# Kernel tuning notes

Measured on AMD Instinct MI355X. Metric: run time of the kernel, lower is better.

## Reference

```python
import jax, jax.numpy as jnp
import numpy as np

H = 1024  # projected hidden size per branch


def setup_inputs() -> dict:
    key = jax.random.key(0)
    ks = jax.random.split(key, 8)
    B, E, D, F = 8, 1024, 1024, 768
    s = 1.0 / np.sqrt(F)
    return {
        "encoder_last_hidden_state": jax.random.normal(ks[0], (B, E, F), jnp.float32),
        "decoder_hidden_states": jax.random.normal(ks[1], (1, B, D, F), jnp.float32),
        "encoder_mask": jnp.ones((B, E), jnp.float32),
        "decoder_mask": jnp.ones((B, D), jnp.float32),
        "W_e": jax.random.normal(ks[2], (H, F), jnp.float32) * s,
        "b_e": jnp.zeros((H,), jnp.float32),
        "W_d": jax.random.normal(ks[3], (H, F), jnp.float32) * s,
        "b_d": jnp.zeros((H,), jnp.float32),
        "W1": jax.random.normal(ks[4], (3, 2 * H), jnp.float32) * (1.0 / np.sqrt(2 * H)),
        "b1": jnp.zeros((3,), jnp.float32),
        "grid_label": jax.random.randint(ks[5], (B, D, E), 0, 3, jnp.int64),
    }


def reference(encoder_last_hidden_state, decoder_hidden_states, encoder_mask,
              decoder_mask, W_e, b_e, W_d, b_d, W1, b1, grid_label):
    # dropout is identity in eval mode
    dec_hs = decoder_hidden_states[-1]                      # (B, D, 768)
    enc_s = jax.nn.relu(encoder_last_hidden_state @ W_e.T + b_e) * encoder_mask[:, :, None]  # (B,E,H)
    dec_s = jax.nn.relu(dec_hs @ W_d.T + b_d) * decoder_mask[:, :, None]                     # (B,D,H)
    # layer_1 on cat([decode, encode], -1) == split GEMMs + broadcast add
    W1_d, W1_e = W1[:, :H], W1[:, H:]
    d_proj = dec_s @ W1_d.T                                 # (B, D, 3)
    e_proj = enc_s @ W1_e.T                                 # (B, E, 3)
    logits = d_proj[:, :, None, :] + e_proj[:, None, :, :] + b1  # (B, D, E, 3)
    logp = jax.nn.log_softmax(logits, axis=-1)
    valid = grid_label != -100
    safe = jnp.where(valid, grid_label, 0)
    nll = -jnp.take_along_axis(logp, safe[..., None].astype(jnp.int32), axis=-1)[..., 0]
    denom = jnp.maximum(jnp.sum(valid.astype(logp.dtype)), 1.0)
    return jnp.sum(jnp.where(valid, nll, 0.0)) / denom
```

## Files before the change

kernel.cpp:

```cpp
#include <hip/hip_runtime.h>
#include <hip/hip_bf16.h>

typedef __attribute__((ext_vector_type(8))) __bf16 bf16x8;
typedef __attribute__((ext_vector_type(4))) float f32x4;

#define HID 1024
#define FD  768
#define MR  8192
#define BM  128
#define BN  128
#define BK  32
#define KSTEPS (FD / BK)

#define GLOAD_LDS16(g, l)                                                  \
    __builtin_amdgcn_global_load_lds(                                      \
        (const __attribute__((address_space(1))) unsigned int*)(g),        \
        (__attribute__((address_space(3))) unsigned int*)(l), 16, 0, 0)

__global__ __launch_bounds__(256)
void cvt_kernel(const float* __restrict__ se, const float* __restrict__ sd,
                const float* __restrict__ swe, const float* __restrict__ swd,
                __bf16* __restrict__ de, __bf16* __restrict__ dd,
                __bf16* __restrict__ dwe, __bf16* __restrict__ dwd)
{
    const int blk = blockIdx.x;
    const float* __restrict__ src;
    __bf16* __restrict__ dst;
    long base;
    if (blk < 3072)      { src = se;  dst = de;  base = (long)blk * 2048; }
    else if (blk < 6144) { src = sd;  dst = dd;  base = (long)(blk - 3072) * 2048; }
    else if (blk < 6528) { src = swe; dst = dwe; base = (long)(blk - 6144) * 2048; }
    else                 { src = swd; dst = dwd; base = (long)(blk - 6528) * 2048; }
    const long i = base + (long)threadIdx.x * 8;
    const float4 a = *reinterpret_cast<const float4*>(src + i);
    const float4 b = *reinterpret_cast<const float4*>(src + i + 4);
    bf16x8 w;
    w[0] = (__bf16)a.x; w[1] = (__bf16)a.y; w[2] = (__bf16)a.z; w[3] = (__bf16)a.w;
    w[4] = (__bf16)b.x; w[5] = (__bf16)b.y; w[6] = (__bf16)b.z; w[7] = (__bf16)b.w;
    *reinterpret_cast<bf16x8*>(dst + i) = w;
}

__global__ __launch_bounds__(256)
void gemm_proj_kernel(const __bf16* __restrict__ Xe, const __bf16* __restrict__ Xd,
                      const __bf16* __restrict__ We, const __bf16* __restrict__ Wd,
                      const float* __restrict__ me, const float* __restrict__ md,
                      const float* __restrict__ be, const float* __restrict__ bd,
                      const float* __restrict__ W1,
                      float* __restrict__ pe, float* __restrict__ pd)
{
    const int z = blockIdx.z;
    const __bf16* __restrict__ X    = z ? Xd : Xe;
    const __bf16* __restrict__ Wt   = z ? Wd : We;
    const float* __restrict__ bias  = z ? bd : be;
    const float* __restrict__ msk   = z ? md : me;
    float* __restrict__ proj        = z ? pd : pe;
    const int w1off = z ? 0 : HID;

    __shared__ union {
        struct { __bf16 A[2][BM][BK]; __bf16 B[2][BN][BK]; } st;
        f32x4 red[BM][16];
    } sm;

    const int t    = threadIdx.x;
    const int lane = t & 63;
    const int wid  = t >> 6;
    const int wr   = wid >> 1;
    const int wc   = wid & 1;
    const int l15  = lane & 15;
    const int l4   = lane >> 4;

    const long m0 = (long)blockIdx.x * BM;
    const int  n0 = blockIdx.y * BN;

    f32x4 acc[4][4];
    #pragma unroll
    for (int i = 0; i < 4; ++i)
        #pragma unroll
        for (int j = 0; j < 4; ++j)
            acc[i][j] = (f32x4){0.f, 0.f, 0.f, 0.f};

    const int srow = lane >> 2;
    const int scol = (lane & 3) * 8;
    const __bf16* ga = X  + (m0 + wid*32 + srow) * (long)FD + scol;
    const __bf16* gb = Wt + (long)(n0 + wid*32 + srow) * FD + scol;

#define STAGE(p, ks) do {                                                  \
        const int k0_ = (ks) * BK;                                         \
        GLOAD_LDS16(ga + k0_,               &sm.st.A[p][wid*32 +  0][0]);  \
        GLOAD_LDS16(ga + (long)16*FD + k0_, &sm.st.A[p][wid*32 + 16][0]);  \
        GLOAD_LDS16(gb + k0_,               &sm.st.B[p][wid*32 +  0][0]);  \
        GLOAD_LDS16(gb + (long)16*FD + k0_, &sm.st.B[p][wid*32 + 16][0]);  \
    } while (0)

    STAGE(0, 0);
    __syncthreads();

    int cur = 0;
    for (int ks = 0; ks < KSTEPS; ++ks) {
        if (ks + 1 < KSTEPS) STAGE(cur ^ 1, ks + 1);

        bf16x8 af[4], bfr[4];
        #pragma unroll
        for (int m = 0; m < 4; ++m)
            af[m] = *reinterpret_cast<const bf16x8*>(&sm.st.A[cur][wr*64 + m*16 + l15][l4*8]);
        #pragma unroll
        for (int n = 0; n < 4; ++n)
            bfr[n] = *reinterpret_cast<const bf16x8*>(&sm.st.B[cur][wc*64 + n*16 + l15][l4*8]);

        #pragma unroll
        for (int m = 0; m < 4; ++m)
            #pragma unroll
            for (int n = 0; n < 4; ++n)
                acc[m][n] = __builtin_amdgcn_mfma_f32_16x16x32_bf16(
                                af[m], bfr[n], acc[m][n], 0, 0, 0);

        __syncthreads();
        cur ^= 1;
    }

    float bh[4], w1c0[4], w1c1[4], w1c2[4];
    #pragma unroll
    for (int n = 0; n < 4; ++n) {
        int h = n0 + wc*64 + n*16 + l15;
        bh[n]   = bias[h];
        w1c0[n] = W1[0*2*HID + w1off + h];
        w1c1[n] = W1[1*2*HID + w1off + h];
        w1c2[n] = W1[2*2*HID + w1off + h];
    }

    #pragma unroll
    for (int pass = 0; pass < 2; ++pass) {
        if (wc == pass) {
            #pragma unroll
            for (int m = 0; m < 4; ++m) {
                #pragma unroll
                for (int r = 0; r < 4; ++r) {
                    float p0 = 0.f, p1 = 0.f, p2 = 0.f;
                    #pragma unroll
                    for (int n = 0; n < 4; ++n) {
                        float s = fmaxf(acc[m][n][r] + bh[n], 0.f);
                        p0 = fmaf(s, w1c0[n], p0);
                        p1 = fmaf(s, w1c1[n], p1);
                        p2 = fmaf(s, w1c2[n], p2);
                    }
                    const int row = wr*64 + m*16 + l4*4 + r;
                    f32x4 v = (f32x4){p0, p1, p2, 0.f};
                    if (pass == 0) sm.red[row][l15] = v;
                    else           sm.red[row][l15] = sm.red[row][l15] + v;
                }
            }
        }
        __syncthreads();
    }

    {
        const int rrow = t >> 1, half = t & 1;
        f32x4 s = (f32x4){0.f, 0.f, 0.f, 0.f};
        #pragma unroll
        for (int j = 0; j < 8; ++j)
            s = s + sm.red[rrow][half*8 + ((j + rrow) & 7)];
        s.x += __shfl_xor(s.x, 1);
        s.y += __shfl_xor(s.y, 1);
        s.z += __shfl_xor(s.z, 1);
        if (half == 0) {
            const long grow = m0 + rrow;
            const float mk = msk[grow];
            atomicAdd(&proj[grow*3+0], s.x * mk);
            atomicAdd(&proj[grow*3+1], s.y * mk);
            atomicAdd(&proj[grow*3+2], s.z * mk);
        }
    }
#undef STAGE
}

__global__ __launch_bounds__(256)
void loss_kernel(const float* __restrict__ pe, const float* __restrict__ pd,
                 const float* __restrict__ b1, const int* __restrict__ labels,
                 float* __restrict__ psum, float* __restrict__ pcnt)
{
    const int g = blockIdx.x;
    const int b = g >> 8;
    const int dbase = (g & 255) * 4;
    const int t = threadIdx.x;
    const int e0 = t * 4;

    const float4* pep = reinterpret_cast<const float4*>(pe + ((long)b*1024 + e0)*3);
    float4 q0 = pep[0], q1 = pep[1], q2 = pep[2];
    float epv[12] = {q0.x,q0.y,q0.z,q0.w, q1.x,q1.y,q1.z,q1.w, q2.x,q2.y,q2.z,q2.w};

    float lsum = 0.f, lcnt = 0.f;
    #pragma unroll
    for (int r = 0; r < 4; ++r) {
        const long bd = (long)b*1024 + dbase + r;
        const float d0 = pd[bd*3+0] + b1[0];
        const float d1 = pd[bd*3+1] + b1[1];
        const float d2 = pd[bd*3+2] + b1[2];
        const int4 lb = *reinterpret_cast<const int4*>(labels + bd*1024 + e0);
        const int lv[4] = {lb.x, lb.y, lb.z, lb.w};
        #pragma unroll
        for (int i = 0; i < 4; ++i) {
            float l0 = d0 + epv[i*3+0];
            float l1 = d1 + epv[i*3+1];
            float l2 = d2 + epv[i*3+2];
            float mx  = fmaxf(l0, fmaxf(l1, l2));
            float lse = mx + __logf(__expf(l0-mx) + __expf(l1-mx) + __expf(l2-mx));
            int la = lv[i];
            if (la != -100) {
                float sel = (la == 0) ? l0 : ((la == 1) ? l1 : l2);
                lsum += lse - sel;
                lcnt += 1.f;
            }
        }
    }
    #pragma unroll
    for (int off = 1; off < 64; off <<= 1) {
        lsum += __shfl_xor(lsum, off);
        lcnt += __shfl_xor(lcnt, off);
    }
    __shared__ float shs[4], shc[4];
    const int wv = t >> 6;
    if ((t & 63) == 0) { shs[wv] = lsum; shc[wv] = lcnt; }
    __syncthreads();
    if (t == 0) {
        psum[g] = shs[0]+shs[1]+shs[2]+shs[3];
        pcnt[g] = shc[0]+shc[1]+shc[2]+shc[3];
    }
}

__global__ __launch_bounds__(256)
void finalize_kernel(const float* __restrict__ psum, const float* __restrict__ pcnt,
                     float* __restrict__ out)
{
    const int t = threadIdx.x;
    float s = 0.f, c = 0.f;
    for (int i = t; i < 2048; i += 256) { s += psum[i]; c += pcnt[i]; }
    #pragma unroll
    for (int off = 1; off < 64; off <<= 1) {
        s += __shfl_xor(s, off);
        c += __shfl_xor(c, off);
    }
    __shared__ float shs[4], shc[4];
    const int wv = t >> 6;
    if ((t & 63) == 0) { shs[wv] = s; shc[wv] = c; }
    __syncthreads();
    if (t == 0)
        out[0] = (shs[0]+shs[1]+shs[2]+shs[3]) / fmaxf(shc[0]+shc[1]+shc[2]+shc[3], 1.0f);
}

extern "C" void kernel_launch(void* const* d_in, const int* in_sizes, int n_in,
                              void* d_out, int out_size, void* d_ws, size_t ws_size,
                              hipStream_t stream)
{
    (void)in_sizes; (void)n_in; (void)out_size; (void)ws_size;

    const float* enc   = (const float*)d_in[0];
    const float* dec   = (const float*)d_in[1];
    const float* maske = (const float*)d_in[2];
    const float* maskd = (const float*)d_in[3];
    const float* We    = (const float*)d_in[4];
    const float* be    = (const float*)d_in[5];
    const float* Wd    = (const float*)d_in[6];
    const float* bd    = (const float*)d_in[7];
    const float* W1    = (const float*)d_in[8];
    const float* b1    = (const float*)d_in[9];
    const int*   labels= (const int*)d_in[10];

    float* pe   = (float*)d_ws;
    float* pd   = pe + 3*MR;
    float* psum = pd + 3*MR;
    float* pcnt = psum + MR;
    __bf16* Xeb = (__bf16*)(pcnt + MR);
    __bf16* Xdb = Xeb + (long)MR*FD;
    __bf16* Web = Xdb + (long)MR*FD;
    __bf16* Wdb = Web + (long)HID*FD;

    hipMemsetAsync(d_ws, 0, (size_t)(6*MR) * sizeof(float), stream);

    cvt_kernel<<<6912, 256, 0, stream>>>(enc, dec, We, Wd, Xeb, Xdb, Web, Wdb);

    dim3 grid(MR/BM, HID/BN, 2);
    gemm_proj_kernel<<<grid, 256, 0, stream>>>(Xeb, Xdb, Web, Wdb,
                                               maske, maskd, be, bd, W1, pe, pd);
    loss_kernel<<<2048, 256, 0, stream>>>(pe, pd, b1, labels, psum, pcnt);
    finalize_kernel<<<1, 256, 0, stream>>>(psum, pcnt, (float*)d_out);
}
```

Before: 181.4 us.

## Use 256x128 GEMM tiles with 512 threads and shuffle-based epilogue reduction

```diff
diff --git a/kernel.cpp b/kernel.cpp
--- a/kernel.cpp
+++ b/kernel.cpp
@@ -7,7 +7,7 @@
 #define HID 1024
 #define FD  768
 #define MR  8192
-#define BM  128
+#define BM  256
 #define BN  128
 #define BK  32
 #define KSTEPS (FD / BK)
@@ -40,7 +40,7 @@
     *reinterpret_cast<bf16x8*>(dst + i) = w;
 }
 
-__global__ __launch_bounds__(256)
+__global__ __launch_bounds__(512, 2)
 void gemm_proj_kernel(const __bf16* __restrict__ Xe, const __bf16* __restrict__ Xd,
                       const __bf16* __restrict__ We, const __bf16* __restrict__ Wd,
                       const float* __restrict__ me, const float* __restrict__ md,
@@ -58,7 +58,7 @@
 
     __shared__ union {
         struct { __bf16 A[2][BM][BK]; __bf16 B[2][BN][BK]; } st;
-        f32x4 red[BM][16];
+        f32x4 red[BM][2];
     } sm;
 
     const int t    = threadIdx.x;
@@ -82,14 +82,13 @@
     const int srow = lane >> 2;
     const int scol = (lane & 3) * 8;
     const __bf16* ga = X  + (m0 + wid*32 + srow) * (long)FD + scol;
-    const __bf16* gb = Wt + (long)(n0 + wid*32 + srow) * FD + scol;
+    const __bf16* gb = Wt + (long)(n0 + wid*16 + srow) * FD + scol;
 
 #define STAGE(p, ks) do {                                                  \
         const int k0_ = (ks) * BK;                                         \
         GLOAD_LDS16(ga + k0_,               &sm.st.A[p][wid*32 +  0][0]);  \
         GLOAD_LDS16(ga + (long)16*FD + k0_, &sm.st.A[p][wid*32 + 16][0]);  \
-        GLOAD_LDS16(gb + k0_,               &sm.st.B[p][wid*32 +  0][0]);  \
-        GLOAD_LDS16(gb + (long)16*FD + k0_, &sm.st.B[p][wid*32 + 16][0]);  \
+        GLOAD_LDS16(gb + k0_,               &sm.st.B[p][wid*16][0]);       \
     } while (0)
 
     STAGE(0, 0);
@@ -129,46 +128,36 @@
     }
 
     #pragma unroll
-    for (int pass = 0; pass < 2; ++pass) {
-        if (wc == pass) {
+    for (int m = 0; m < 4; ++m) {
+        #pragma unroll
+        for (int r = 0; r < 4; ++r) {
+            float p0 = 0.f, p1 = 0.f, p2 = 0.f;
             #pragma unroll
-            for (int m = 0; m < 4; ++m) {
-                #pragma unroll
-                for (int r = 0; r < 4; ++r) {
-                    float p0 = 0.f, p1 = 0.f, p2 = 0.f;
-                    #pragma unroll
-                    for (int n = 0; n < 4; ++n) {
-                        float s = fmaxf(acc[m][n][r] + bh[n], 0.f);
-                        p0 = fmaf(s, w1c0[n], p0);
-                        p1 = fmaf(s, w1c1[n], p1);
-                        p2 = fmaf(s, w1c2[n], p2);
-                    }
-                    const int row = wr*64 + m*16 + l4*4 + r;
-                    f32x4 v = (f32x4){p0, p1, p2, 0.f};
-                    if (pass == 0) sm.red[row][l15] = v;
-                    else           sm.red[row][l15] = sm.red[row][l15] + v;
-                }
+            for (int n = 0; n < 4; ++n) {
+                float s = fmaxf(acc[m][n][r] + bh[n], 0.f);
+                p0 = fmaf(s, w1c0[n], p0);
+                p1 = fmaf(s, w1c1[n], p1);
+                p2 = fmaf(s, w1c2[n], p2);
             }
+            #pragma unroll
+            for (int off = 1; off < 16; off <<= 1) {
+                p0 += __shfl_xor(p0, off);
+                p1 += __shfl_xor(p1, off);
+                p2 += __shfl_xor(p2, off);
+            }
+            if (l15 == 0)
+                sm.red[wr*64 + m*16 + l4*4 + r][wc] = (f32x4){p0, p1, p2, 0.f};
         }
-        __syncthreads();
-    }
-
-    {
-        const int rrow = t >> 1, half = t & 1;
-        f32x4 s = (f32x4){0.f, 0.f, 0.f, 0.f};
-        #pragma unroll
-        for (int j = 0; j < 8; ++j)
-            s = s + sm.red[rrow][half*8 + ((j + rrow) & 7)];
-        s.x += __shfl_xor(s.x, 1);
-        s.y += __shfl_xor(s.y, 1);
-        s.z += __shfl_xor(s.z, 1);
-        if (half == 0) {
-            const long grow = m0 + rrow;
-            const float mk = msk[grow];
-            atomicAdd(&proj[grow*3+0], s.x * mk);
-            atomicAdd(&proj[grow*3+1], s.y * mk);
-            atomicAdd(&proj[grow*3+2], s.z * mk);
-        }
+    }
+    __syncthreads();
+
+    if (t < BM) {
+        f32x4 s = sm.red[t][0] + sm.red[t][1];
+        const long grow = m0 + t;
+        const float mk = msk[grow];
+        atomicAdd(&proj[grow*3+0], s.x * mk);
+        atomicAdd(&proj[grow*3+1], s.y * mk);
+        atomicAdd(&proj[grow*3+2], s.z * mk);
     }
 #undef STAGE
 }
@@ -279,7 +268,7 @@
     cvt_kernel<<<6912, 256, 0, stream>>>(enc, dec, We, Wd, Xeb, Xdb, Web, Wdb);
 
     dim3 grid(MR/BM, HID/BN, 2);
-    gemm_proj_kernel<<<grid, 256, 0, stream>>>(Xeb, Xdb, Web, Wdb,
+    gemm_proj_kernel<<<grid, 512, 0, stream>>>(Xeb, Xdb, Web, Wdb,
                                                maske, maskd, be, bd, W1, pe, pd);
     loss_kernel<<<2048, 256, 0, stream>>>(pe, pd, b1, labels, psum, pcnt);
     finalize_kernel<<<1, 256, 0, stream>>>(psum, pcnt, (float*)d_out);
```

New measurement: 181.8 us. About the same (+0.2%).
